# Kernel optimization log

Measured on AMD Instinct MI355X. Metric: run time of the kernel, lower is better.

Reference implementation:

```python
import math
import jax, jax.numpy as jnp
import numpy as np

B, N, TOKEN_DIM = 8, 8192, 512
NODE_DIM = 64
MAX_NODES = 64
SCORE_HIDDEN = 64


def setup_inputs() -> dict:
    key = jax.random.key(0)
    ks = jax.random.split(key, 8)
    s = lambda k, shape, fan_in: jax.random.normal(k, shape, jnp.float32) / np.sqrt(fan_in)
    return {
        "token_feats": jax.random.normal(ks[0], (B, N, TOKEN_DIM), jnp.float32),
        "score_w1": s(ks[1], (TOKEN_DIM, SCORE_HIDDEN), TOKEN_DIM),
        "score_b1": jnp.zeros((SCORE_HIDDEN,), jnp.float32),
        "score_w2": s(ks[2], (SCORE_HIDDEN, 1), SCORE_HIDDEN),
        "score_b2": jnp.zeros((1,), jnp.float32),
        "t2n_w": s(ks[3], (TOKEN_DIM, NODE_DIM), TOKEN_DIM),
        "n2t_w": s(ks[4], (NODE_DIM, TOKEN_DIM), NODE_DIM),
        "gcn_w1": s(ks[5], (NODE_DIM, NODE_DIM), NODE_DIM),
        "gcn_w2": s(ks[6], (NODE_DIM, NODE_DIM), NODE_DIM),
    }


def reference(token_feats, score_w1, score_b1, score_w2, score_b2,
              t2n_w, n2t_w, gcn_w1, gcn_w2):
    Bn, Nn, d = token_feats.shape
    M = MAX_NODES
    eps = 1e-6

    # --- node selection (scores -> threshold -> top-k among selected) ---
    h = jax.nn.relu(jnp.einsum('bnd,dh->bnh', token_feats, score_w1) + score_b1)
    scores = (jnp.einsum('bnh,ho->bno', h, score_w2) + score_b2)[..., 0]  # [B,N]
    mean = scores.mean(axis=1, keepdims=True)
    std = scores.std(axis=1, keepdims=True)  # unbiased=False (population)
    thr = mean + 0.5 * std
    count = jnp.sum(scores > thr, axis=1)  # [B]
    fallback_k = min(M, max(4, Nn // 16))
    take_k = jnp.where(count == 0, fallback_k, jnp.minimum(count, M))  # [B]

    _, top_idx = jax.lax.top_k(scores, M)  # [B,M] highest scores; set == torch's selection
    node_mask = jnp.arange(M)[None, :] < take_k[:, None]  # [B,M] bool
    maskf = node_mask.astype(token_feats.dtype)

    gathered = jnp.take_along_axis(token_feats, top_idx[..., None], axis=1)  # [B,M,d]
    H0 = jnp.einsum('bmd,dk->bmk', gathered, t2n_w) * maskf[..., None]  # [B,M,node_dim]

    # --- cosine-similarity adjacency, masked, self-loops, row-normalized ---
    nrm = jnp.maximum(jnp.linalg.norm(H0, axis=-1, keepdims=True), eps)
    Hn = H0 / nrm
    A = jax.nn.relu(jnp.einsum('bik,bjk->bij', Hn, Hn))
    A = A * (maskf[:, :, None] * maskf[:, None, :])
    A = A + jnp.eye(M, dtype=A.dtype)[None] * maskf[:, None, :]
    A = A / jnp.maximum(A.sum(axis=-1, keepdims=True), 1e-6)

    # --- two-layer GCN (no bias) ---
    x = jax.nn.relu(jnp.einsum('bij,bjk,kl->bil', A, H0, gcn_w1))
    Hg = jax.nn.relu(jnp.einsum('bij,bjk,kl->bil', A, x, gcn_w2))  # [B,M,node_dim]

    # --- attention scatter-back to tokens ---
    token_proj = jnp.einsum('bnd,dk->bnk', token_feats, t2n_w)  # [B,N,node_dim]
    logits = jnp.einsum('bnk,bmk->bnm', token_proj, Hg) / math.sqrt(NODE_DIM)
    attn = jax.nn.softmax(logits, axis=-1)
    injected = jnp.einsum('bnm,bmk->bnk', attn, Hg)
    back = jnp.einsum('bnk,kd->bnd', injected, n2t_w)
    return token_feats + back
```

## Files before the change

kernel.cpp:

```cpp
#include <hip/hip_runtime.h>
#include <hip/hip_bf16.h>

#define B_ 8
#define N_ 8192
#define D_ 512
#define M_ 64

typedef unsigned short u16;
typedef unsigned int u32;
typedef __attribute__((ext_vector_type(8))) short bf16x8;
typedef __attribute__((ext_vector_type(4))) float f32x4;

__device__ __forceinline__ u16 f2bf(float f) {
  u32 u = __float_as_uint(f);
  u += 0x7FFFu + ((u >> 16) & 1u);
  return (u16)(u >> 16);
}
__device__ __forceinline__ float bf2f(u16 h) {
  return __uint_as_float(((u32)h) << 16);
}

__device__ __forceinline__ int bfrag_idx(int kd, int c, int ncols16) {
  int sub = (kd >> 5) * ncols16 + (c >> 4);
  int lane = (c & 15) + 16 * ((kd & 15) >> 2);
  int e = (kd & 3) + 4 * ((kd >> 4) & 1);
  return sub * 512 + lane * 8 + e;
}

__device__ __forceinline__ int kslot(int ln, int e) {
  return (e & 3) + 4 * (ln >> 4) + 16 * (e >> 2);
}

__device__ __forceinline__ bf16x8 pack8(float4 v0, float4 v1) {
  bf16x8 a;
  a[0] = (short)f2bf(v0.x); a[1] = (short)f2bf(v0.y);
  a[2] = (short)f2bf(v0.z); a[3] = (short)f2bf(v0.w);
  a[4] = (short)f2bf(v1.x); a[5] = (short)f2bf(v1.y);
  a[6] = (short)f2bf(v1.z); a[7] = (short)f2bf(v1.w);
  return a;
}

__global__ __launch_bounds__(256) void k_prep(
    const float* __restrict__ t2n, const float* __restrict__ n2t,
    const float* __restrict__ W1, const float* __restrict__ g1,
    const float* __restrict__ g2,
    u16* __restrict__ t2nf, u16* __restrict__ n2tf,
    u16* __restrict__ W1h, u16* __restrict__ W1l,
    u16* __restrict__ g1f, u16* __restrict__ g2f)
{
  const int gid = blockIdx.x * 256 + threadIdx.x;
  const int stride = gridDim.x * 256;
  for (int s = gid; s < 512 * 64; s += stride) {
    const int k = s >> 6, c = s & 63;
    const int idx = bfrag_idx(k, c, 4);
    t2nf[idx] = f2bf(t2n[s]);
    const float w = W1[s];
    const u16 wh = f2bf(w);
    W1h[idx] = wh;
    W1l[idx] = f2bf(w - bf2f(wh));
  }
  for (int s = gid; s < 64 * 512; s += stride) {
    const int k = s >> 9, c = s & 511;
    n2tf[bfrag_idx(k, c, 32)] = f2bf(n2t[s]);
  }
  for (int s = gid; s < 4096; s += stride) {
    const int k = s >> 6, c = s & 63;
    g1f[bfrag_idx(k, c, 4)] = f2bf(g1[s]);
    g2f[bfrag_idx(k, c, 4)] = f2bf(g2[s]);
  }
}

__global__ __launch_bounds__(256, 4) void k_sp(
    const float* __restrict__ X, const u16* __restrict__ W1h,
    const u16* __restrict__ W1l, const u16* __restrict__ t2nf,
    const float* __restrict__ b1, const float* __restrict__ w2,
    const float* __restrict__ b2, float* __restrict__ scores,
    float* __restrict__ outStash)
{
  __shared__ __align__(16) u16 sB[2][6144];
  __shared__ __align__(16) u16 sAf[4096];
  const int tid = threadIdx.x;
  const int t0 = blockIdx.x * 64;
  const int wv = tid >> 6, ln = tid & 63;
  const int lq = ln >> 4, lr = ln & 15;
  u16* mySf = &sAf[wv * 1024];
  const float* xr = X + (size_t)(t0 + 16 * wv + lr) * D_;

  f32x4 acc[4], accP[4];
  #pragma unroll
  for (int cb = 0; cb < 4; ++cb) {
    acc[cb] = (f32x4){0.f, 0.f, 0.f, 0.f};
    accP[cb] = (f32x4){0.f, 0.f, 0.f, 0.f};
  }

  auto gsrc = [&](int f, int kb) -> const u16* {
    const int cb = f / 3, mat = f % 3;
    const u16* mp = (mat == 0) ? W1h : (mat == 1) ? W1l : t2nf;
    return mp + (kb * 4 + cb) * 512 + ln * 8;
  };

  bf16x8 wr[3];
  #pragma unroll
  for (int j = 0; j < 3; ++j)
    *(bf16x8*)&sB[0][(j * 4 + wv) * 512 + ln * 8] = *(const bf16x8*)gsrc(j * 4 + wv, 0);
  #pragma unroll
  for (int j = 0; j < 3; ++j) wr[j] = *(const bf16x8*)gsrc(j * 4 + wv, 1);
  float4 va0 = *(const float4*)(xr + 4 * lq);
  float4 va1 = *(const float4*)(xr + 16 + 4 * lq);
  __syncthreads();

  for (int kb = 0; kb < 16; ++kb) {
    const int cur = kb & 1;
    if (kb < 15) {
      #pragma unroll
      for (int j = 0; j < 3; ++j)
        *(bf16x8*)&sB[cur ^ 1][(j * 4 + wv) * 512 + ln * 8] = wr[j];
    }
    if (kb < 14) {
      #pragma unroll
      for (int j = 0; j < 3; ++j) wr[j] = *(const bf16x8*)gsrc(j * 4 + wv, kb + 2);
    }
    const float4 v0 = va0, v1 = va1;
    if (kb < 15) {
      va0 = *(const float4*)(xr + 32 * (kb + 1) + 4 * lq);
      va1 = *(const float4*)(xr + 32 * (kb + 1) + 16 + 4 * lq);
    }
    const float xs[8] = {v0.x, v0.y, v0.z, v0.w, v1.x, v1.y, v1.z, v1.w};
    bf16x8 ah, al;
    #pragma unroll
    for (int e = 0; e < 8; ++e) {
      const u16 h = f2bf(xs[e]);
      ah[e] = (short)h;
      al[e] = (short)f2bf(xs[e] - bf2f(h));
    }
    #pragma unroll
    for (int cb = 0; cb < 4; ++cb) {
      const bf16x8 bh = *(const bf16x8*)&sB[cur][(cb * 3 + 0) * 512 + ln * 8];
      const bf16x8 bl = *(const bf16x8*)&sB[cur][(cb * 3 + 1) * 512 + ln * 8];
      const bf16x8 bt = *(const bf16x8*)&sB[cur][(cb * 3 + 2) * 512 + ln * 8];
      acc[cb]  = __builtin_amdgcn_mfma_f32_16x16x32_bf16(ah, bh, acc[cb], 0, 0, 0);
      acc[cb]  = __builtin_amdgcn_mfma_f32_16x16x32_bf16(ah, bl, acc[cb], 0, 0, 0);
      acc[cb]  = __builtin_amdgcn_mfma_f32_16x16x32_bf16(al, bh, acc[cb], 0, 0, 0);
      accP[cb] = __builtin_amdgcn_mfma_f32_16x16x32_bf16(ah, bt, accP[cb], 0, 0, 0);
    }
    __syncthreads();
  }

  float b1v[4], w2v[4];
  #pragma unroll
  for (int cb = 0; cb < 4; ++cb) {
    const int col = cb * 16 + lr;
    b1v[cb] = b1[col]; w2v[cb] = w2[col];
  }
  const float b2v = b2[0];
  #pragma unroll
  for (int r = 0; r < 4; ++r) {
    float p = 0.f;
    #pragma unroll
    for (int cb = 0; cb < 4; ++cb) {
      const float h = fmaxf(acc[cb][r] + b1v[cb], 0.f);
      p = fmaf(h, w2v[cb], p);
    }
    p += __shfl_xor(p, 1); p += __shfl_xor(p, 2);
    p += __shfl_xor(p, 4); p += __shfl_xor(p, 8);
    if (lr == 0) scores[t0 + wv * 16 + 4 * lq + r] = p + b2v;
  }

  #pragma unroll
  for (int cb = 0; cb < 4; ++cb)
    #pragma unroll
    for (int r = 0; r < 4; ++r) {
      const int idx = (cb >> 1) * 512 + (4 * lq + r + 16 * (lr >> 2)) * 8 +
                      (lr & 3) + 4 * (cb & 1);
      mySf[idx] = f2bf(accP[cb][r]);
    }
  u16* stash = (u16*)(outStash + (size_t)blockIdx.x * 32768);
  #pragma unroll
  for (int kb2 = 0; kb2 < 2; ++kb2)
    *(bf16x8*)&stash[wv * 1024 + kb2 * 512 + ln * 8] =
        *(const bf16x8*)&mySf[kb2 * 512 + ln * 8];
}

__global__ __launch_bounds__(1024) void k_select(
    const float* __restrict__ scores, int* __restrict__ top_idx,
    int* __restrict__ take_k)
{
  __shared__ u32 hist[256];
  __shared__ float redf[34];
  __shared__ u32 redu[16];
  __shared__ u32 sPrefix, sRank, sCntA, sCntT;
  __shared__ int candIdx[64];
  __shared__ float candVal[64];
  __shared__ int tieIdx[128];
  const int b = blockIdx.x, tid = threadIdx.x;
  const int wv = tid >> 6, ln = tid & 63;
  const float* s = scores + (size_t)b * N_;

  float v[8]; u32 key[8];
  float sum = 0.f, sq = 0.f;
  #pragma unroll
  for (int j = 0; j < 8; ++j) {
    v[j] = s[tid + j * 1024];
    sum += v[j]; sq = fmaf(v[j], v[j], sq);
    const u32 u = __float_as_uint(v[j]);
    key[j] = u ^ ((u32)((int)u >> 31) | 0x80000000u);
  }
  if (tid < 256) hist[tid] = 0;
  #pragma unroll
  for (int off = 32; off > 0; off >>= 1) {
    sum += __shfl_xor(sum, off);
    sq  += __shfl_xor(sq, off);
  }
  if (ln == 0) { redf[wv] = sum; redf[16 + wv] = sq; }
  __syncthreads();
  if (tid < 16) {
    float a = redf[tid], q = redf[16 + tid];
    #pragma unroll
    for (int off = 8; off > 0; off >>= 1) {
      a += __shfl_down(a, off);
      q += __shfl_down(q, off);
    }
    if (tid == 0) {
      const float mean = a / (float)N_;
      const float var = q / (float)N_ - mean * mean;
      redf[32] = mean + 0.5f * sqrtf(fmaxf(var, 0.f));
    }
  }
  __syncthreads();
  const float thr = redf[32];

  int c = 0;
  #pragma unroll
  for (int j = 0; j < 8; ++j) {
    c += (v[j] > thr) ? 1 : 0;
    atomicAdd(&hist[key[j] >> 24], 1u);
  }
  #pragma unroll
  for (int off = 32; off > 0; off >>= 1) c += __shfl_xor(c, off);
  if (ln == 0) redu[wv] = (u32)c;
  __syncthreads();
  if (tid < 16) {
    u32 a = redu[tid];
    #pragma unroll
    for (int off = 8; off > 0; off >>= 1) a += (u32)__shfl_down((int)a, off);
    if (tid == 0) {
      const int cnt = (int)a;
      take_k[b] = (cnt == 0) ? M_ : (cnt < M_ ? cnt : M_);
    }
  }

  u32 prefix = 0, rank = 64, pmask = 0;
  for (int pass = 0; pass < 4; ++pass) {
    const int shift = 24 - 8 * pass;
    if (pass > 0) {
      if (tid < 256) hist[tid] = 0;
      __syncthreads();
      #pragma unroll
      for (int j = 0; j < 8; ++j)
        if ((key[j] & pmask) == prefix) atomicAdd(&hist[(key[j] >> shift) & 255u], 1u);
      __syncthreads();
    }
    if (tid < 64) {
      const u32 h0 = hist[4 * tid], h1 = hist[4 * tid + 1];
      const u32 h2 = hist[4 * tid + 2], h3 = hist[4 * tid + 3];
      const u32 s3 = h3, s2 = h2 + s3, s1 = h1 + s2, s0 = h0 + s1;
      u32 run = s0;
      #pragma unroll
      for (int off = 1; off < 64; off <<= 1) {
        const u32 t = (u32)__shfl_down((int)run, off);
        if (tid + off < 64) run += t;
      }
      const u32 excl = run - s0;
      const u32 c0 = s0 + excl, c1 = s1 + excl, c2 = s2 + excl, c3 = s3 + excl;
      int pick = -1; u32 nxt = 0;
      if (c0 >= rank && c1 < rank)        { pick = 0; nxt = c1; }
      else if (c1 >= rank && c2 < rank)   { pick = 1; nxt = c2; }
      else if (c2 >= rank && c3 < rank)   { pick = 2; nxt = c3; }
      else if (c3 >= rank && excl < rank) { pick = 3; nxt = excl; }
      if (pick >= 0) {
        sPrefix = prefix | ((u32)(4 * tid + pick) << shift);
        sRank = rank - nxt;
      }
    }
    __syncthreads();
    prefix = sPrefix; rank = sRank;
    pmask |= 0xFFu << shift;
    __syncthreads();
  }

  if (tid == 0) { sCntA = 0; sCntT = 0; }
  __syncthreads();
  const u32 pivot = prefix;
  #pragma unroll
  for (int j = 0; j < 8; ++j) {
    if (key[j] > pivot) {
      const u32 p = atomicAdd(&sCntA, 1u);
      candIdx[p] = tid + j * 1024; candVal[p] = v[j];
    } else if (key[j] == pivot) {
      const u32 p = atomicAdd(&sCntT, 1u);
      if (p < 128) tieIdx[p] = tid + j * 1024;
    }
  }
  __syncthreads();
  if (tid == 0) {
    const int nA = (int)sCntA;
    const int need = 64 - nA;
    int nT = (int)sCntT; if (nT > 128) nT = 128;
    const float pv = (pivot & 0x80000000u)
                         ? __uint_as_float(pivot ^ 0x80000000u)
                         : __uint_as_float(~pivot);
    for (int j = 0; j < need; ++j) {
      int bi = 1 << 30, bp = -1;
      for (int q = 0; q < nT; ++q) {
        const int vv = tieIdx[q];
        if (vv >= 0 && vv < bi) { bi = vv; bp = q; }
      }
      candIdx[nA + j] = bi; candVal[nA + j] = pv; tieIdx[bp] = -1;
    }
  }
  __syncthreads();
  if (tid < 64) {
    const float vv = candVal[tid]; const int ii = candIdx[tid];
    int rk = 0;
    for (int j = 0; j < 64; ++j) {
      const float vj = candVal[j]; const int ij = candIdx[j];
      rk += (vj > vv || (vj == vv && ij < ii)) ? 1 : 0;
    }
    top_idx[b * M_ + rk] = ii;
  }
}

__device__ __forceinline__ bf16x8 ldsA_frag(const float (*S)[65], int wv, int kb, int ln) {
  const int lr = ln & 15;
  bf16x8 a;
  #pragma unroll
  for (int e = 0; e < 8; ++e) a[e] = (short)f2bf(S[16 * wv + lr][32 * kb + kslot(ln, e)]);
  return a;
}
__device__ __forceinline__ bf16x8 ldsB_frag(const float (*S)[65], int cb, int kb, int ln) {
  const int lr = ln & 15;
  bf16x8 bb;
  #pragma unroll
  for (int e = 0; e < 8; ++e) bb[e] = (short)f2bf(S[32 * kb + kslot(ln, e)][16 * cb + lr]);
  return bb;
}
__device__ __forceinline__ bf16x8 ldsBT_frag(const float (*S)[65], int cb, int kb, int ln) {
  const int lr = ln & 15;
  bf16x8 bb;
  #pragma unroll
  for (int e = 0; e < 8; ++e) bb[e] = (short)f2bf(S[16 * cb + lr][32 * kb + kslot(ln, e)]);
  return bb;
}

__global__ __launch_bounds__(256) void k_graph(
    const float* __restrict__ X, const u16* __restrict__ t2nf,
    const u16* __restrict__ n2tf, const u16* __restrict__ g1f,
    const u16* __restrict__ g2f, const int* __restrict__ top_idx,
    const int* __restrict__ take_k, u16* __restrict__ HgTf,
    u16* __restrict__ Wf)
{
  __shared__ float sH0[64][65];
  __shared__ float sA[64][65];
  __shared__ float sT[64][65];
  __shared__ float sU[64][65];
  __shared__ float sR[64];
  const int b = blockIdx.x, tid = threadIdx.x;
  const int wv = tid >> 6, ln = tid & 63;
  const int lq = ln >> 4, lr = ln & 15;
  const int tk = take_k[b];
  const int rowm = 16 * wv + 4 * lq;

  const int gidx = top_idx[b * M_ + 16 * wv + lr];
  const float* xr = X + ((size_t)b * N_ + gidx) * D_;
  f32x4 d[4];
  #pragma unroll
  for (int cb = 0; cb < 4; ++cb) d[cb] = (f32x4){0.f, 0.f, 0.f, 0.f};
  {
    float4 p0[3], p1[3];
    #pragma unroll
    for (int q = 0; q < 3; ++q) {
      p0[q] = *(const float4*)(xr + 32 * q + 4 * lq);
      p1[q] = *(const float4*)(xr + 32 * q + 16 + 4 * lq);
    }
    #pragma unroll
    for (int kb = 0; kb < 16; ++kb) {
      const int slot = kb % 3;
      const float4 v0 = p0[slot], v1 = p1[slot];
      if (kb + 3 < 16) {
        p0[slot] = *(const float4*)(xr + 32 * (kb + 3) + 4 * lq);
        p1[slot] = *(const float4*)(xr + 32 * (kb + 3) + 16 + 4 * lq);
      }
      const bf16x8 a = pack8(v0, v1);
      #pragma unroll
      for (int cb = 0; cb < 4; ++cb) {
        const bf16x8 bb = *(const bf16x8*)&t2nf[(kb * 4 + cb) * 512 + ln * 8];
        d[cb] = __builtin_amdgcn_mfma_f32_16x16x32_bf16(a, bb, d[cb], 0, 0, 0);
      }
    }
  }
  #pragma unroll
  for (int cb = 0; cb < 4; ++cb)
    #pragma unroll
    for (int r = 0; r < 4; ++r)
      sH0[rowm + r][16 * cb + lr] = (rowm + r < tk) ? d[cb][r] : 0.f;
  __syncthreads();

  if (tid < 64) {
    float ss = 0.f;
    #pragma unroll
    for (int k = 0; k < 64; ++k) { const float vv = sH0[tid][k]; ss = fmaf(vv, vv, ss); }
    sR[tid] = 1.f / fmaxf(sqrtf(ss), 1e-6f);
  }
  __syncthreads();
  #pragma unroll
  for (int p = 0; p < 16; ++p) {
    const int o = tid + p * 256;
    sU[o >> 6][o & 63] = sH0[o >> 6][o & 63] * sR[o >> 6];
  }
  __syncthreads();

  #pragma unroll
  for (int cb = 0; cb < 4; ++cb) d[cb] = (f32x4){0.f, 0.f, 0.f, 0.f};
  #pragma unroll
  for (int kb = 0; kb < 2; ++kb) {
    const bf16x8 a = ldsA_frag(sU, wv, kb, ln);
    #pragma unroll
    for (int cb = 0; cb < 4; ++cb)
      d[cb] = __builtin_amdgcn_mfma_f32_16x16x32_bf16(a, ldsBT_frag(sU, cb, kb, ln), d[cb], 0, 0, 0);
  }
  __syncthreads();
  #pragma unroll
  for (int cb = 0; cb < 4; ++cb)
    #pragma unroll
    for (int r = 0; r < 4; ++r) {
      const int row = rowm + r, col = 16 * cb + lr;
      float ss = fmaxf(d[cb][r], 0.f);
      ss = (row < tk && col < tk) ? ss : 0.f;
      if (row == col && row < tk) ss += 1.f;
      sA[row][col] = ss;
    }
  __syncthreads();

  if (tid < 64) {
    float rs = 0.f;
    #pragma unroll
    for (int j = 0; j < 64; ++j) rs += sA[tid][j];
    sR[tid] = 1.f / fmaxf(rs, 1e-6f);
  }
  __syncthreads();
  #pragma unroll
  for (int p = 0; p < 16; ++p) {
    const int o = tid + p * 256;
    sA[o >> 6][o & 63] *= sR[o >> 6];
  }
  __syncthreads();

  #pragma unroll
  for (int cb = 0; cb < 4; ++cb) d[cb] = (f32x4){0.f, 0.f, 0.f, 0.f};
  #pragma unroll
  for (int kb = 0; kb < 2; ++kb) {
    const bf16x8 a = ldsA_frag(sA, wv, kb, ln);
    #pragma unroll
    for (int cb = 0; cb < 4; ++cb)
      d[cb] = __builtin_amdgcn_mfma_f32_16x16x32_bf16(a, ldsB_frag(sH0, cb, kb, ln), d[cb], 0, 0, 0);
  }
  __syncthreads();
  #pragma unroll
  for (int cb = 0; cb < 4; ++cb)
    #pragma unroll
    for (int r = 0; r < 4; ++r) sT[rowm + r][16 * cb + lr] = d[cb][r];
  __syncthreads();

  #pragma unroll
  for (int cb = 0; cb < 4; ++cb) d[cb] = (f32x4){0.f, 0.f, 0.f, 0.f};
  #pragma unroll
  for (int kb = 0; kb < 2; ++kb) {
    const bf16x8 a = ldsA_frag(sT, wv, kb, ln);
    #pragma unroll
    for (int cb = 0; cb < 4; ++cb) {
      const bf16x8 bb = *(const bf16x8*)&g1f[(kb * 4 + cb) * 512 + ln * 8];
      d[cb] = __builtin_amdgcn_mfma_f32_16x16x32_bf16(a, bb, d[cb], 0, 0, 0);
    }
  }
  __syncthreads();
  #pragma unroll
  for (int cb = 0; cb < 4; ++cb)
    #pragma unroll
    for (int r = 0; r < 4; ++r) sU[rowm + r][16 * cb + lr] = fmaxf(d[cb][r], 0.f);
  __syncthreads();

  #pragma unroll
  for (int cb = 0; cb < 4; ++cb) d[cb] = (f32x4){0.f, 0.f, 0.f, 0.f};
  #pragma unroll
  for (int kb = 0; kb < 2; ++kb) {
    const bf16x8 a = ldsA_frag(sA, wv, kb, ln);
    #pragma unroll
    for (int cb = 0; cb < 4; ++cb)
      d[cb] = __builtin_amdgcn_mfma_f32_16x16x32_bf16(a, ldsB_frag(sU, cb, kb, ln), d[cb], 0, 0, 0);
  }
  __syncthreads();
  #pragma unroll
  for (int cb = 0; cb < 4; ++cb)
    #pragma unroll
    for (int r = 0; r < 4; ++r) sT[rowm + r][16 * cb + lr] = d[cb][r];
  __syncthreads();

  #pragma unroll
  for (int cb = 0; cb < 4; ++cb) d[cb] = (f32x4){0.f, 0.f, 0.f, 0.f};
  #pragma unroll
  for (int kb = 0; kb < 2; ++kb) {
    const bf16x8 a = ldsA_frag(sT, wv, kb, ln);
    #pragma unroll
    for (int cb = 0; cb < 4; ++cb) {
      const bf16x8 bb = *(const bf16x8*)&g2f[(kb * 4 + cb) * 512 + ln * 8];
      d[cb] = __builtin_amdgcn_mfma_f32_16x16x32_bf16(a, bb, d[cb], 0, 0, 0);
    }
  }
  __syncthreads();
  #pragma unroll
  for (int cb = 0; cb < 4; ++cb)
    #pragma unroll
    for (int r = 0; r < 4; ++r) {
      const int node = rowm + r, feat = 16 * cb + lr;
      const float hv = fmaxf(d[cb][r], 0.f);
      HgTf[(size_t)b * 4096 + bfrag_idx(feat, node, 4)] = f2bf(hv);
      sU[node][feat] = hv;
    }
  __syncthreads();

  for (int chk = 0; chk < 4; ++chk) {
    f32x4 aw[8];
    #pragma unroll
    for (int c8 = 0; c8 < 8; ++c8) aw[c8] = (f32x4){0.f, 0.f, 0.f, 0.f};
    #pragma unroll
    for (int kbf = 0; kbf < 2; ++kbf) {
      const bf16x8 a = ldsA_frag(sU, wv, kbf, ln);
      #pragma unroll
      for (int c8 = 0; c8 < 8; ++c8) {
        const bf16x8 bb = *(const bf16x8*)&n2tf[(kbf * 32 + chk * 8 + c8) * 512 + ln * 8];
        aw[c8] = __builtin_amdgcn_mfma_f32_16x16x32_bf16(a, bb, aw[c8], 0, 0, 0);
      }
    }
    #pragma unroll
    for (int c8 = 0; c8 < 8; ++c8)
      #pragma unroll
      for (int r = 0; r < 4; ++r) {
        const int m = 16 * wv + 4 * lq + r;
        const int cc = (chk * 8 + c8) * 16 + lr;
        Wf[(size_t)b * 32768 + bfrag_idx(m, cc, 32)] = f2bf(aw[c8][r]);
      }
  }
}

__global__ __launch_bounds__(256) void k_attn(
    const float* __restrict__ X, const u16* __restrict__ HgTf,
    const u16* __restrict__ Wf, float* __restrict__ out)
{
  __shared__ __align__(16) u16 sAf[4096];
  __shared__ __align__(16) float sBo[4][16][68];
  const int tid = threadIdx.x;
  const int b = blockIdx.x >> 7;
  const int t0 = (blockIdx.x & 127) << 6;
  const float* Xb = X + (size_t)b * N_ * D_;
  float* Ob = out + (size_t)b * N_ * D_;
  const int wv = tid >> 6, ln = tid & 63;
  const int lq = ln >> 4, lr = ln & 15;
  u16* mySf = &sAf[wv * 1024];
  const u16* stash = (const u16*)(out + (size_t)blockIdx.x * 32768);

  f32x4 accL[4];
  #pragma unroll
  for (int cb = 0; cb < 4; ++cb) accL[cb] = (f32x4){0.f, 0.f, 0.f, 0.f};
  #pragma unroll
  for (int kb = 0; kb < 2; ++kb) {
    const bf16x8 a = *(const bf16x8*)&stash[wv * 1024 + kb * 512 + ln * 8];
    #pragma unroll
    for (int cb = 0; cb < 4; ++cb) {
      const bf16x8 bb = *(const bf16x8*)&HgTf[(size_t)b * 4096 + (kb * 4 + cb) * 512 + ln * 8];
      accL[cb] = __builtin_amdgcn_mfma_f32_16x16x32_bf16(a, bb, accL[cb], 0, 0, 0);
    }
  }
  __syncthreads();

  float attnv[4][4];
  #pragma unroll
  for (int r = 0; r < 4; ++r) {
    const float v0 = accL[0][r], v1 = accL[1][r], v2 = accL[2][r], v3 = accL[3][r];
    float mx = fmaxf(fmaxf(v0, v1), fmaxf(v2, v3));
    mx = fmaxf(mx, __shfl_xor(mx, 1)); mx = fmaxf(mx, __shfl_xor(mx, 2));
    mx = fmaxf(mx, __shfl_xor(mx, 4)); mx = fmaxf(mx, __shfl_xor(mx, 8));
    const float e0 = __expf((v0 - mx) * 0.125f), e1 = __expf((v1 - mx) * 0.125f);
    const float e2 = __expf((v2 - mx) * 0.125f), e3 = __expf((v3 - mx) * 0.125f);
    float sm = (e0 + e1) + (e2 + e3);
    sm += __shfl_xor(sm, 1); sm += __shfl_xor(sm, 2);
    sm += __shfl_xor(sm, 4); sm += __shfl_xor(sm, 8);
    const float inv = 1.f / sm;
    attnv[0][r] = e0 * inv; attnv[1][r] = e1 * inv;
    attnv[2][r] = e2 * inv; attnv[3][r] = e3 * inv;
  }
  #pragma unroll
  for (int cb = 0; cb < 4; ++cb)
    #pragma unroll
    for (int r = 0; r < 4; ++r) {
      const int idx = (cb >> 1) * 512 + (4 * lq + r + 16 * (lr >> 2)) * 8 +
                      (lr & 3) + 4 * (cb & 1);
      mySf[idx] = f2bf(attnv[cb][r]);
    }

  for (int chk = 0; chk < 4; ++chk) {
    float4 xres[8];
    #pragma unroll
    for (int h = 0; h < 2; ++h)
      #pragma unroll
      for (int j = 0; j < 4; ++j)
        xres[h * 4 + j] = *(const float4*)(
            Xb + (size_t)(t0 + 16 * wv + 4 * j + lq) * D_ + chk * 128 + h * 64 + 4 * lr);

    f32x4 accB[8];
    #pragma unroll
    for (int c8 = 0; c8 < 8; ++c8) accB[c8] = (f32x4){0.f, 0.f, 0.f, 0.f};
    #pragma unroll
    for (int kb = 0; kb < 2; ++kb) {
      const bf16x8 a = *(const bf16x8*)&mySf[kb * 512 + ln * 8];
      #pragma unroll
      for (int c8 = 0; c8 < 8; ++c8) {
        const bf16x8 bb = *(const bf16x8*)&Wf[(size_t)b * 32768 + (kb * 32 + chk * 8 + c8) * 512 + ln * 8];
        accB[c8] = __builtin_amdgcn_mfma_f32_16x16x32_bf16(a, bb, accB[c8], 0, 0, 0);
      }
    }
    #pragma unroll
    for (int h = 0; h < 2; ++h) {
      #pragma unroll
      for (int c4 = 0; c4 < 4; ++c4)
        #pragma unroll
        for (int r = 0; r < 4; ++r)
          sBo[wv][4 * lq + r][c4 * 16 + lr] = accB[4 * h + c4][r];
      #pragma unroll
      for (int j = 0; j < 4; ++j) {
        const int rloc = 4 * j + lq;
        float4 vv = *(const float4*)&sBo[wv][rloc][4 * lr];
        const float4 xv = xres[h * 4 + j];
        vv.x += xv.x; vv.y += xv.y; vv.z += xv.z; vv.w += xv.w;
        *(float4*)(Ob + (size_t)(t0 + 16 * wv + rloc) * D_ + chk * 128 + h * 64 + 4 * lr) = vv;
      }
    }
  }
}

extern "C" void kernel_launch(void* const* d_in, const int* in_sizes, int n_in,
                              void* d_out, int out_size, void* d_ws, size_t ws_size,
                              hipStream_t stream)
{
  (void)in_sizes; (void)n_in; (void)out_size; (void)ws_size;
  const float* X   = (const float*)d_in[0];
  const float* W1  = (const float*)d_in[1];
  const float* b1  = (const float*)d_in[2];
  const float* w2  = (const float*)d_in[3];
  const float* b2  = (const float*)d_in[4];
  const float* t2n = (const float*)d_in[5];
  const float* n2t = (const float*)d_in[6];
  const float* g1  = (const float*)d_in[7];
  const float* g2  = (const float*)d_in[8];
  float* out = (float*)d_out;

  char* ws = (char*)d_ws;
  float* scores = (float*)(ws);
  u16* t2nf     = (u16*)(ws + 262144);
  u16* n2tf     = (u16*)(ws + 327680);
  u16* W1h      = (u16*)(ws + 393216);
  u16* W1l      = (u16*)(ws + 458752);
  u16* HgTf     = (u16*)(ws + 524288);
  u16* g1f      = (u16*)(ws + 589824);
  u16* g2f      = (u16*)(ws + 598016);
  int* top_idx  = (int*)(ws + 606208);
  int* take_k   = (int*)(ws + 608256);
  u16* Wf       = (u16*)(ws + 609280);

  k_prep<<<64, 256, 0, stream>>>(t2n, n2t, W1, g1, g2, t2nf, n2tf, W1h, W1l, g1f, g2f);
  k_sp<<<1024, 256, 0, stream>>>(X, W1h, W1l, t2nf, b1, w2, b2, scores, out);
  k_select<<<B_, 1024, 0, stream>>>(scores, top_idx, take_k);
  k_graph<<<B_, 256, 0, stream>>>(X, t2nf, n2tf, g1f, g2f, top_idx, take_k, HgTf, Wf);
  k_attn<<<1024, 256, 0, stream>>>(X, HgTf, Wf, out);
}
```

Baseline: 127.8 us.

## Single-pass 11-bit radix top-k select and split graph kernel across 8 waves

The top-k selection kernel drops its four-pass 8-bit radix refinement in favour of one 2048-bin histogram on the top 11 key bits. Elements in the pivot bin are then ranked in parallel by key and index, replacing the serial single-thread tie resolution. The graph kernel now runs with 512 threads, and each wave computes half of the output column blocks, so its serial per-batch work is spread over twice as many waves. This relies on the pivot bin holding at most 1024 elements, and adds a quadratic parallel rank pass over that bin.

```diff
diff --git a/kernel.cpp b/kernel.cpp
--- a/kernel.cpp
+++ b/kernel.cpp
@@ -185,16 +185,22 @@
     const float* __restrict__ scores, int* __restrict__ top_idx,
     int* __restrict__ take_k)
 {
-  __shared__ u32 hist[256];
+  __shared__ u32 hist[2048];
   __shared__ float redf[34];
   __shared__ u32 redu[16];
-  __shared__ u32 sPrefix, sRank, sCntA, sCntT;
+  __shared__ u32 scanp[16];
+  __shared__ int sPivotBin;
+  __shared__ u32 sTake, sNA, sCntA, sCntT;
   __shared__ int candIdx[64];
-  __shared__ float candVal[64];
-  __shared__ int tieIdx[128];
+  __shared__ u32 candKey[64];
+  __shared__ int tieIdx[1024];
+  __shared__ u32 tieKey[1024];
   const int b = blockIdx.x, tid = threadIdx.x;
   const int wv = tid >> 6, ln = tid & 63;
   const float* s = scores + (size_t)b * N_;
+
+  hist[tid] = 0; hist[tid + 1024] = 0;
+  if (tid == 0) { sCntA = 0; sCntT = 0; }
 
   float v[8]; u32 key[8];
   float sum = 0.f, sq = 0.f;
@@ -205,7 +211,6 @@
     const u32 u = __float_as_uint(v[j]);
     key[j] = u ^ ((u32)((int)u >> 31) | 0x80000000u);
   }
-  if (tid < 256) hist[tid] = 0;
   #pragma unroll
   for (int off = 32; off > 0; off >>= 1) {
     sum += __shfl_xor(sum, off);
@@ -213,6 +218,9 @@
   }
   if (ln == 0) { redf[wv] = sum; redf[16 + wv] = sq; }
   __syncthreads();
+
+  #pragma unroll
+  for (int j = 0; j < 8; ++j) atomicAdd(&hist[key[j] >> 21], 1u);
   if (tid < 16) {
     float a = redf[tid], q = redf[16 + tid];
     #pragma unroll
@@ -231,14 +239,22 @@
 
   int c = 0;
   #pragma unroll
-  for (int j = 0; j < 8; ++j) {
-    c += (v[j] > thr) ? 1 : 0;
-    atomicAdd(&hist[key[j] >> 24], 1u);
-  }
+  for (int j = 0; j < 8; ++j) c += (v[j] > thr) ? 1 : 0;
   #pragma unroll
   for (int off = 32; off > 0; off >>= 1) c += __shfl_xor(c, off);
   if (ln == 0) redu[wv] = (u32)c;
-  __syncthreads();
+
+  const u32 h_hi = hist[2 * tid], h_lo = hist[2 * tid + 1];
+  const u32 ps = h_hi + h_lo;
+  u32 run = ps;
+  #pragma unroll
+  for (int off = 1; off < 64; off <<= 1) {
+    const u32 t = (u32)__shfl((int)run, ln + off);
+    if (ln + off < 64) run += t;
+  }
+  if (ln == 0) scanp[wv] = run;
+  __syncthreads();
+
   if (tid < 16) {
     u32 a = redu[tid];
     #pragma unroll
@@ -248,93 +264,65 @@
       take_k[b] = (cnt == 0) ? M_ : (cnt < M_ ? cnt : M_);
     }
   }
-
-  u32 prefix = 0, rank = 64, pmask = 0;
-  for (int pass = 0; pass < 4; ++pass) {
-    const int shift = 24 - 8 * pass;
-    if (pass > 0) {
-      if (tid < 256) hist[tid] = 0;
-      __syncthreads();
-      #pragma unroll
-      for (int j = 0; j < 8; ++j)
-        if ((key[j] & pmask) == prefix) atomicAdd(&hist[(key[j] >> shift) & 255u], 1u);
-      __syncthreads();
-    }
-    if (tid < 64) {
-      const u32 h0 = hist[4 * tid], h1 = hist[4 * tid + 1];
-      const u32 h2 = hist[4 * tid + 2], h3 = hist[4 * tid + 3];
-      const u32 s3 = h3, s2 = h2 + s3, s1 = h1 + s2, s0 = h0 + s1;
-      u32 run = s0;
-      #pragma unroll
-      for (int off = 1; off < 64; off <<= 1) {
-        const u32 t = (u32)__shfl_down((int)run, off);
-        if (tid + off < 64) run += t;
-      }
-      const u32 excl = run - s0;
-      const u32 c0 = s0 + excl, c1 = s1 + excl, c2 = s2 + excl, c3 = s3 + excl;
-      int pick = -1; u32 nxt = 0;
-      if (c0 >= rank && c1 < rank)        { pick = 0; nxt = c1; }
-      else if (c1 >= rank && c2 < rank)   { pick = 1; nxt = c2; }
-      else if (c2 >= rank && c3 < rank)   { pick = 2; nxt = c3; }
-      else if (c3 >= rank && excl < rank) { pick = 3; nxt = excl; }
-      if (pick >= 0) {
-        sPrefix = prefix | ((u32)(4 * tid + pick) << shift);
-        sRank = rank - nxt;
-      }
-    }
-    __syncthreads();
-    prefix = sPrefix; rank = sRank;
-    pmask |= 0xFFu << shift;
-    __syncthreads();
-  }
-
-  if (tid == 0) { sCntA = 0; sCntT = 0; }
-  __syncthreads();
-  const u32 pivot = prefix;
+  {
+    u32 ws = 0;
+    for (int w = wv + 1; w < 16; ++w) ws += scanp[w];
+    const u32 suffIncl = run + ws;
+    const u32 cumMid = suffIncl - h_hi;
+    const u32 cumNext = suffIncl - ps;
+    if (suffIncl >= 64u && cumMid < 64u) {
+      sPivotBin = 2 * tid; sTake = 64u - cumMid; sNA = cumMid;
+    }
+    if (cumMid >= 64u && cumNext < 64u) {
+      sPivotBin = 2 * tid + 1; sTake = 64u - cumNext; sNA = cumNext;
+    }
+  }
+  __syncthreads();
+
+  const int pb = sPivotBin;
   #pragma unroll
   for (int j = 0; j < 8; ++j) {
-    if (key[j] > pivot) {
+    const int bin = (int)(key[j] >> 21);
+    if (bin > pb) {
       const u32 p = atomicAdd(&sCntA, 1u);
-      candIdx[p] = tid + j * 1024; candVal[p] = v[j];
-    } else if (key[j] == pivot) {
+      candIdx[p] = tid + j * 1024; candKey[p] = key[j];
+    } else if (bin == pb) {
       const u32 p = atomicAdd(&sCntT, 1u);
-      if (p < 128) tieIdx[p] = tid + j * 1024;
-    }
-  }
-  __syncthreads();
-  if (tid == 0) {
-    const int nA = (int)sCntA;
-    const int need = 64 - nA;
-    int nT = (int)sCntT; if (nT > 128) nT = 128;
-    const float pv = (pivot & 0x80000000u)
-                         ? __uint_as_float(pivot ^ 0x80000000u)
-                         : __uint_as_float(~pivot);
-    for (int j = 0; j < need; ++j) {
-      int bi = 1 << 30, bp = -1;
-      for (int q = 0; q < nT; ++q) {
-        const int vv = tieIdx[q];
-        if (vv >= 0 && vv < bi) { bi = vv; bp = q; }
-      }
-      candIdx[nA + j] = bi; candVal[nA + j] = pv; tieIdx[bp] = -1;
-    }
-  }
-  __syncthreads();
+      if (p < 1024u) { tieIdx[p] = tid + j * 1024; tieKey[p] = key[j]; }
+    }
+  }
+  __syncthreads();
+
+  const int nA = (int)sNA;
+  const int need = (int)sTake;
+  const int T = (int)(sCntT < 1024u ? sCntT : 1024u);
+  for (int t = tid; t < T; t += 1024) {
+    const u32 k0 = tieKey[t]; const int i0 = tieIdx[t];
+    int rk = 0;
+    for (int q = 0; q < T; ++q) {
+      const u32 kq = tieKey[q]; const int iq = tieIdx[q];
+      rk += (kq > k0 || (kq == k0 && iq < i0)) ? 1 : 0;
+    }
+    if (rk < need) { candIdx[nA + rk] = i0; candKey[nA + rk] = k0; }
+  }
+  __syncthreads();
+
   if (tid < 64) {
-    const float vv = candVal[tid]; const int ii = candIdx[tid];
+    const u32 k0 = candKey[tid]; const int i0 = candIdx[tid];
     int rk = 0;
-    for (int j = 0; j < 64; ++j) {
-      const float vj = candVal[j]; const int ij = candIdx[j];
-      rk += (vj > vv || (vj == vv && ij < ii)) ? 1 : 0;
-    }
-    top_idx[b * M_ + rk] = ii;
-  }
-}
-
-__device__ __forceinline__ bf16x8 ldsA_frag(const float (*S)[65], int wv, int kb, int ln) {
+    for (int q = 0; q < 64; ++q) {
+      const u32 kq = candKey[q]; const int iq = candIdx[q];
+      rk += (kq > k0 || (kq == k0 && iq < i0)) ? 1 : 0;
+    }
+    top_idx[b * M_ + rk] = i0;
+  }
+}
+
+__device__ __forceinline__ bf16x8 ldsA_frag(const float (*S)[65], int g, int kb, int ln) {
   const int lr = ln & 15;
   bf16x8 a;
   #pragma unroll
-  for (int e = 0; e < 8; ++e) a[e] = (short)f2bf(S[16 * wv + lr][32 * kb + kslot(ln, e)]);
+  for (int e = 0; e < 8; ++e) a[e] = (short)f2bf(S[16 * g + lr][32 * kb + kslot(ln, e)]);
   return a;
 }
 __device__ __forceinline__ bf16x8 ldsB_frag(const float (*S)[65], int cb, int kb, int ln) {
@@ -352,7 +340,7 @@
   return bb;
 }
 
-__global__ __launch_bounds__(256) void k_graph(
+__global__ __launch_bounds__(512) void k_graph(
     const float* __restrict__ X, const u16* __restrict__ t2nf,
     const u16* __restrict__ n2tf, const u16* __restrict__ g1f,
     const u16* __restrict__ g2f, const int* __restrict__ top_idx,
@@ -367,14 +355,16 @@
   const int b = blockIdx.x, tid = threadIdx.x;
   const int wv = tid >> 6, ln = tid & 63;
   const int lq = ln >> 4, lr = ln & 15;
+  const int g = wv & 3;
+  const int hh = wv >> 2;
   const int tk = take_k[b];
-  const int rowm = 16 * wv + 4 * lq;
-
-  const int gidx = top_idx[b * M_ + 16 * wv + lr];
+  const int rowm = 16 * g + 4 * lq;
+
+  const int gidx = top_idx[b * M_ + 16 * g + lr];
   const float* xr = X + ((size_t)b * N_ + gidx) * D_;
-  f32x4 d[4];
-  #pragma unroll
-  for (int cb = 0; cb < 4; ++cb) d[cb] = (f32x4){0.f, 0.f, 0.f, 0.f};
+  f32x4 d[2];
+  #pragma unroll
+  for (int cc = 0; cc < 2; ++cc) d[cc] = (f32x4){0.f, 0.f, 0.f, 0.f};
   {
     float4 p0[3], p1[3];
     #pragma unroll
@@ -392,17 +382,18 @@
       }
       const bf16x8 a = pack8(v0, v1);
       #pragma unroll
-      for (int cb = 0; cb < 4; ++cb) {
+      for (int cc = 0; cc < 2; ++cc) {
+        const int cb = 2 * hh + cc;
         const bf16x8 bb = *(const bf16x8*)&t2nf[(kb * 4 + cb) * 512 + ln * 8];
-        d[cb] = __builtin_amdgcn_mfma_f32_16x16x32_bf16(a, bb, d[cb], 0, 0, 0);
+        d[cc] = __builtin_amdgcn_mfma_f32_16x16x32_bf16(a, bb, d[cc], 0, 0, 0);
       }
     }
   }
   #pragma unroll
-  for (int cb = 0; cb < 4; ++cb)
+  for (int cc = 0; cc < 2; ++cc)
     #pragma unroll
     for (int r = 0; r < 4; ++r)
-      sH0[rowm + r][16 * cb + lr] = (rowm + r < tk) ? d[cb][r] : 0.f;
+      sH0[rowm + r][16 * (2 * hh + cc) + lr] = (rowm + r < tk) ? d[cc][r] : 0.f;
   __syncthreads();
 
   if (tid < 64) {
@@ -413,28 +404,28 @@
   }
   __syncthreads();
   #pragma unroll
-  for (int p = 0; p < 16; ++p) {
-    const int o = tid + p * 256;
+  for (int p = 0; p < 8; ++p) {
+    const int o = tid + p * 512;
     sU[o >> 6][o & 63] = sH0[o >> 6][o & 63] * sR[o >> 6];
   }
   __syncthreads();
 
   #pragma unroll
-  for (int cb = 0; cb < 4; ++cb) d[cb] = (f32x4){0.f, 0.f, 0.f, 0.f};
+  for (int cc = 0; cc < 2; ++cc) d[cc] = (f32x4){0.f, 0.f, 0.f, 0.f};
   #pragma unroll
   for (int kb = 0; kb < 2; ++kb) {
-    const bf16x8 a = ldsA_frag(sU, wv, kb, ln);
-    #pragma unroll
-    for (int cb = 0; cb < 4; ++cb)
-      d[cb] = __builtin_amdgcn_mfma_f32_16x16x32_bf16(a, ldsBT_frag(sU, cb, kb, ln), d[cb], 0, 0, 0);
-  }
-  __syncthreads();
-  #pragma unroll
-  for (int cb = 0; cb < 4; ++cb)
+    const bf16x8 a = ldsA_frag(sU, g, kb, ln);
+    #pragma unroll
+    for (int cc = 0; cc < 2; ++cc)
+      d[cc] = __builtin_amdgcn_mfma_f32_16x16x32_bf16(a, ldsBT_frag(sU, 2 * hh + cc, kb, ln), d[cc], 0, 0, 0);
+  }
+  __syncthreads();
+  #pragma unroll
+  for (int cc = 0; cc < 2; ++cc)
     #pragma unroll
     for (int r = 0; r < 4; ++r) {
-      const int row = rowm + r, col = 16 * cb + lr;
-      float ss = fmaxf(d[cb][r], 0.f);
+      const int row = rowm + r, col = 16 * (2 * hh + cc) + lr;
+      float ss = fmaxf(d[cc][r], 0.f);
       ss = (row < tk && col < tk) ? ss : 0.f;
       if (row == col && row < tk) ss += 1.f;
       sA[row][col] = ss;
@@ -449,92 +440,94 @@
   }
   __syncthreads();
   #pragma unroll
-  for (int p = 0; p < 16; ++p) {
-    const int o = tid + p * 256;
+  for (int p = 0; p < 8; ++p) {
+    const int o = tid + p * 512;
     sA[o >> 6][o & 63] *= sR[o >> 6];
   }
   __syncthreads();
 
   #pragma unroll
-  for (int cb = 0; cb < 4; ++cb) d[cb] = (f32x4){0.f, 0.f, 0.f, 0.f};
+  for (int cc = 0; cc < 2; ++cc) d[cc] = (f32x4){0.f, 0.f, 0.f, 0.f};
   #pragma unroll
   for (int kb = 0; kb < 2; ++kb) {
-    const bf16x8 a = ldsA_frag(sA, wv, kb, ln);
-    #pragma unroll
-    for (int cb = 0; cb < 4; ++cb)
-      d[cb] = __builtin_amdgcn_mfma_f32_16x16x32_bf16(a, ldsB_frag(sH0, cb, kb, ln), d[cb], 0, 0, 0);
-  }
-  __syncthreads();
-  #pragma unroll
-  for (int cb = 0; cb < 4; ++cb)
-    #pragma unroll
-    for (int r = 0; r < 4; ++r) sT[rowm + r][16 * cb + lr] = d[cb][r];
-  __syncthreads();
-
-  #pragma unroll
-  for (int cb = 0; cb < 4; ++cb) d[cb] = (f32x4){0.f, 0.f, 0.f, 0.f};
+    const bf16x8 a = ldsA_frag(sA, g, kb, ln);
+    #pragma unroll
+    for (int cc = 0; cc < 2; ++cc)
+      d[cc] = __builtin_amdgcn_mfma_f32_16x16x32_bf16(a, ldsB_frag(sH0, 2 * hh + cc, kb, ln), d[cc], 0, 0, 0);
+  }
+  __syncthreads();
+  #pragma unroll
+  for (int cc = 0; cc < 2; ++cc)
+    #pragma unroll
+    for (int r = 0; r < 4; ++r) sT[rowm + r][16 * (2 * hh + cc) + lr] = d[cc][r];
+  __syncthreads();
+
+  #pragma unroll
+  for (int cc = 0; cc < 2; ++cc) d[cc] = (f32x4){0.f, 0.f, 0.f, 0.f};
   #pragma unroll
   for (int kb = 0; kb < 2; ++kb) {
-    const bf16x8 a = ldsA_frag(sT, wv, kb, ln);
-    #pragma unroll
-    for (int cb = 0; cb < 4; ++cb) {
-      const bf16x8 bb = *(const bf16x8*)&g1f[(kb * 4 + cb) * 512 + ln * 8];
-      d[cb] = __builtin_amdgcn_mfma_f32_16x16x32_bf16(a, bb, d[cb], 0, 0, 0);
-    }
-  }
-  __syncthreads();
-  #pragma unroll
-  for (int cb = 0; cb < 4; ++cb)
-    #pragma unroll
-    for (int r = 0; r < 4; ++r) sU[rowm + r][16 * cb + lr] = fmaxf(d[cb][r], 0.f);
-  __syncthreads();
-
-  #pragma unroll
-  for (int cb = 0; cb < 4; ++cb) d[cb] = (f32x4){0.f, 0.f, 0.f, 0.f};
+    const bf16x8 a = ldsA_frag(sT, g, kb, ln);
+    #pragma unroll
+    for (int cc = 0; cc < 2; ++cc) {
+      const bf16x8 bb = *(const bf16x8*)&g1f[(kb * 4 + 2 * hh + cc) * 512 + ln * 8];
+      d[cc] = __builtin_amdgcn_mfma_f32_16x16x32_bf16(a, bb, d[cc], 0, 0, 0);
+    }
+  }
+  __syncthreads();
+  #pragma unroll
+  for (int cc = 0; cc < 2; ++cc)
+    #pragma unroll
+    for (int r = 0; r < 4; ++r)
+      sU[rowm + r][16 * (2 * hh + cc) + lr] = fmaxf(d[cc][r], 0.f);
+  __syncthreads();
+
+  #pragma unroll
+  for (int cc = 0; cc < 2; ++cc) d[cc] = (f32x4){0.f, 0.f, 0.f, 0.f};
   #pragma unroll
   for (int kb = 0; kb < 2; ++kb) {
-    const bf16x8 a = ldsA_frag(sA, wv, kb, ln);
-    #pragma unroll
-    for (int cb = 0; cb < 4; ++cb)
-      d[cb] = __builtin_amdgcn_mfma_f32_16x16x32_bf16(a, ldsB_frag(sU, cb, kb, ln), d[cb], 0, 0, 0);
-  }
-  __syncthreads();
-  #pragma unroll
-  for (int cb = 0; cb < 4; ++cb)
-    #pragma unroll
-    for (int r = 0; r < 4; ++r) sT[rowm + r][16 * cb + lr] = d[cb][r];
-  __syncthreads();
-
-  #pragma unroll
-  for (int cb = 0; cb < 4; ++cb) d[cb] = (f32x4){0.f, 0.f, 0.f, 0.f};
+    const bf16x8 a = ldsA_frag(sA, g, kb, ln);
+    #pragma unroll
+    for (int cc = 0; cc < 2; ++cc)
+      d[cc] = __builtin_amdgcn_mfma_f32_16x16x32_bf16(a, ldsB_frag(sU, 2 * hh + cc, kb, ln), d[cc], 0, 0, 0);
+  }
+  __syncthreads();
+  #pragma unroll
+  for (int cc = 0; cc < 2; ++cc)
+    #pragma unroll
+    for (int r = 0; r < 4; ++r) sT[rowm + r][16 * (2 * hh + cc) + lr] = d[cc][r];
+  __syncthreads();
+
+  #pragma unroll
+  for (int cc = 0; cc < 2; ++cc) d[cc] = (f32x4){0.f, 0.f, 0.f, 0.f};
   #pragma unroll
   for (int kb = 0; kb < 2; ++kb) {
-    const bf16x8 a = ldsA_frag(sT, wv, kb, ln);
-    #pragma unroll
-    for (int cb = 0; cb < 4; ++cb) {
-      const bf16x8 bb = *(const bf16x8*)&g2f[(kb * 4 + cb) * 512 + ln * 8];
-      d[cb] = __builtin_amdgcn_mfma_f32_16x16x32_bf16(a, bb, d[cb], 0, 0, 0);
-    }
-  }
-  __syncthreads();
-  #pragma unroll
-  for (int cb = 0; cb < 4; ++cb)
+    const bf16x8 a = ldsA_frag(sT, g, kb, ln);
+    #pragma unroll
+    for (int cc = 0; cc < 2; ++cc) {
+      const bf16x8 bb = *(const bf16x8*)&g2f[(kb * 4 + 2 * hh + cc) * 512 + ln * 8];
+      d[cc] = __builtin_amdgcn_mfma_f32_16x16x32_bf16(a, bb, d[cc], 0, 0, 0);
+    }
+  }
+  __syncthreads();
+  #pragma unroll
+  for (int cc = 0; cc < 2; ++cc)
     #pragma unroll
     for (int r = 0; r < 4; ++r) {
-      const int node = rowm + r, feat = 16 * cb + lr;
-      const float hv = fmaxf(d[cb][r], 0.f);
+      const int node = rowm + r, feat = 16 * (2 * hh + cc) + lr;
+      const float hv = fmaxf(d[cc][r], 0.f);
       HgTf[(size_t)b * 4096 + bfrag_idx(feat, node, 4)] = f2bf(hv);
       sU[node][feat] = hv;
     }
   __syncthreads();
 
-  for (int chk = 0; chk < 4; ++chk) {
+  for (int chkc = 0; chkc < 2; ++chkc) {
+    const int chk = 2 * hh + chkc;
     f32x4 aw[8];
     #pragma unroll
     for (int c8 = 0; c8 < 8; ++c8) aw[c8] = (f32x4){0.f, 0.f, 0.f, 0.f};
     #pragma unroll
     for (int kbf = 0; kbf < 2; ++kbf) {
-      const bf16x8 a = ldsA_frag(sU, wv, kbf, ln);
+      const bf16x8 a = ldsA_frag(sU, g, kbf, ln);
       #pragma unroll
       for (int c8 = 0; c8 < 8; ++c8) {
         const bf16x8 bb = *(const bf16x8*)&n2tf[(kbf * 32 + chk * 8 + c8) * 512 + ln * 8];
@@ -545,9 +538,9 @@
     for (int c8 = 0; c8 < 8; ++c8)
       #pragma unroll
       for (int r = 0; r < 4; ++r) {
-        const int m = 16 * wv + 4 * lq + r;
-        const int cc = (chk * 8 + c8) * 16 + lr;
-        Wf[(size_t)b * 32768 + bfrag_idx(m, cc, 32)] = f2bf(aw[c8][r]);
+        const int m = 16 * g + 4 * lq + r;
+        const int cc2 = (chk * 8 + c8) * 16 + lr;
+        Wf[(size_t)b * 32768 + bfrag_idx(m, cc2, 32)] = f2bf(aw[c8][r]);
       }
   }
 }
@@ -679,6 +672,6 @@
   k_prep<<<64, 256, 0, stream>>>(t2n, n2t, W1, g1, g2, t2nf, n2tf, W1h, W1l, g1f, g2f);
   k_sp<<<1024, 256, 0, stream>>>(X, W1h, W1l, t2nf, b1, w2, b2, scores, out);
   k_select<<<B_, 1024, 0, stream>>>(scores, top_idx, take_k);
-  k_graph<<<B_, 256, 0, stream>>>(X, t2nf, n2tf, g1f, g2f, top_idx, take_k, HgTf, Wf);
+  k_graph<<<B_, 512, 0, stream>>>(X, t2nf, n2tf, g1f, g2f, top_idx, take_k, HgTf, Wf);
   k_attn<<<1024, 256, 0, stream>>>(X, HgTf, Wf, out);
 }
```

Measured after the change: 123.4 us (median of 2 runs). -3.4%, faster.
